# Performance work log

Hardware: AMD Instinct MI355X
Metric: run time of the kernel (lower is better)

Reference implementation:

```python
import jax, jax.numpy as jnp
import numpy as np

B, C, H, W = 4, 512, 64, 64
RED = 2
IC = C // RED  # inter_channels = 256


def _conv1x1(x, w, b):
    # mmcv ConvModule default: conv(+bias) then ReLU
    return jax.nn.relu(jnp.einsum('bchw,oc->bohw', x, w) + b[None, :, None, None])


def setup_inputs() -> dict:
    key = jax.random.key(0)
    ks = jax.random.split(key, 9)
    s_q = 0.02  # small init so exp(-dist) stays in a sane range
    return {
        'features': jax.random.normal(ks[0], (B, C, H, W), jnp.float32),
        'qw': jax.random.normal(ks[1], (IC, C), jnp.float32) * s_q,
        'qb': jnp.zeros((IC,), jnp.float32),
        'kw': jax.random.normal(ks[2], (IC, C), jnp.float32) * s_q,
        'kb': jnp.zeros((IC,), jnp.float32),
        'vw': jax.random.normal(ks[3], (C, C), jnp.float32) * s_q,
        'vb': jnp.zeros((C,), jnp.float32),
        'cw': jax.random.normal(ks[4], (IC, 2), jnp.float32) * s_q,
        'cb': jnp.zeros((IC,), jnp.float32),
    }


def reference(features, qw, qb, kw, kb, vw, vb, cw, cb):
    b, c, h, w = features.shape
    q = _conv1x1(features, qw, qb)   # [b, IC, h, w]
    k = _conv1x1(features, kw, kb)   # [b, IC, h, w]
    v = _conv1x1(features, vw, vb)   # [b, C,  h, w]

    # coordinate grid: channel 0 varies along w, channel 1 along h
    lin = jnp.linspace(-1.0, 1.0, h)
    A = jnp.broadcast_to(lin[None, :], (h, w))
    coord = jnp.broadcast_to(jnp.stack([A, A.T], axis=0)[None], (b, 2, h, w))
    cc = _conv1x1(coord, cw, cb)     # [b, IC, h, w]

    q = q + cc
    k = k + cc

    n = h * w
    Qf = q.reshape(b, -1, n).transpose(0, 2, 1)  # [b, n, IC]
    Kf = k.reshape(b, -1, n)                     # [b, IC, n]

    dots = jnp.einsum('bnc,bcm->bnm', Qf, Kf)    # [b, n, n]
    a_sq = jnp.sum(Qf * Qf, axis=-1)             # [b, n]
    b_sq = jnp.sum(Kf * Kf, axis=1)              # [b, n]
    D = a_sq[:, :, None] + b_sq[:, None, :] - 2.0 * dots
    S = jnp.exp(-D)
    S = S / (jnp.sum(S, axis=-1, keepdims=True) + 1e-14)

    Vf = v.reshape(b, c, n)                      # [b, C, n]
    out = jnp.einsum('bcn,bnm->bcm', Vf, S).reshape(b, c, h, w)
    return out + features
```

## Files before the change

kernel.cpp:

```cpp
#include <hip/hip_runtime.h>
#include <math.h>

#define BATCH 4
#define CH    512
#define ICH   256
#define NPIX  4096

typedef short short8 __attribute__((ext_vector_type(8)));
typedef float floatx4 __attribute__((ext_vector_type(4)));

#define BK   64
#define TS   136

static __device__ __forceinline__ unsigned short f2bf(float x) {
    union { float f; unsigned u; } v; v.f = x;
    unsigned r = (v.u + 0x7FFF + ((v.u >> 16) & 1)) >> 16;
    return (unsigned short)r;
}
static __device__ __forceinline__ float bf2f(unsigned short u) {
    union { unsigned u; float f; } v; v.u = ((unsigned)u) << 16; return v.f;
}
static __device__ __forceinline__ unsigned pack_bf(unsigned ue, unsigned uo) {
    return ((ue + 0x8000u) >> 16) | ((uo + 0x8000u) & 0xFFFF0000u);
}

static __device__ __forceinline__ void gld16(const unsigned short* g, unsigned short* l) {
    __builtin_amdgcn_global_load_lds(
        (const __attribute__((address_space(1))) unsigned int*)g,
        (__attribute__((address_space(3))) unsigned int*)l,
        16, 0, 0);
}

#define STAGE_TILE(L, M, row0, RS, k0)                                        \
    {                                                                         \
        int r_  = (it*32) + wid*8 + (lane >> 3);                              \
        int c_  = (lane & 7) ^ ((lane >> 3) & 7);                             \
        gld16(&(M)[(size_t)((row0) + r_)*(RS) + (k0) + c_*8],                 \
              &(L)[(it*32 + wid*8)*64]);                                      \
    }

#define STG64(L, M, row0, RS, k0, u)                                          \
    {                                                                         \
        int r_  = (u)*64 + wid*8 + (lane >> 3);                               \
        int c_  = (lane & 7) ^ ((lane >> 3) & 7);                             \
        gld16(&(M)[(size_t)((row0) + r_)*(RS) + (k0) + c_*8],                 \
              &(L)[((u)*64 + wid*8)*64]);                                     \
    }

#define FRAG(L, row, ks) \
    (*(const short8*)&(L)[(row)*64 + (((((ks)<<2) + quad) ^ (lo & 7)) << 3)])

__global__ __launch_bounds__(256)
void prep_w(const float* __restrict__ qw, const float* __restrict__ kw,
            const float* __restrict__ vw, unsigned short* __restrict__ Wb)
{
    int i = (blockIdx.x*256 + threadIdx.x) * 4;
    const float* src;
    int off;
    if (i < 256*512)            { src = qw; off = i; }
    else if (i < 512*512)       { src = kw; off = i - 256*512; }
    else                        { src = vw; off = i - 512*512; }
    float4 f = *(const float4*)&src[off];
    unsigned short pk[4] = { f2bf(f.x), f2bf(f.y), f2bf(f.z), f2bf(f.w) };
    *(uint2*)&Wb[i] = *(uint2*)pk;
}

__global__ __launch_bounds__(256)
void prep_ft(const float* __restrict__ feat, unsigned short* __restrict__ Ft)
{
    __shared__ unsigned short S[64][65];
    const int t = threadIdx.x;
    const int n0 = blockIdx.x * 64, c0 = blockIdx.y * 64, b = blockIdx.z;

    #pragma unroll
    for (int rep = 0; rep < 4; rep++) {
        int cl = rep*16 + (t >> 4), col4 = (t & 15) * 4;
        float4 f = *(const float4*)&feat[((size_t)b*CH + c0 + cl)*NPIX + n0 + col4];
        S[cl][col4 + 0] = f2bf(f.x);
        S[cl][col4 + 1] = f2bf(f.y);
        S[cl][col4 + 2] = f2bf(f.z);
        S[cl][col4 + 3] = f2bf(f.w);
    }
    __syncthreads();
    #pragma unroll
    for (int rep = 0; rep < 4; rep++) {
        int nn = rep*16 + (t >> 4), cq = t & 15;
        unsigned short h4[4];
        #pragma unroll
        for (int j = 0; j < 4; j++) h4[j] = S[cq*4 + j][nn];
        *(uint2*)&Ft[((size_t)b*NPIX + n0 + nn)*CH + c0 + cq*4] = *(uint2*)h4;
    }
}

__global__ __launch_bounds__(256)
void conv_mfma(const unsigned short* __restrict__ Ft,
               const unsigned short* __restrict__ Wb,
               const float* __restrict__ qb, const float* __restrict__ kb,
               const float* __restrict__ vb,
               const float* __restrict__ cw, const float* __restrict__ cb,
               unsigned short* __restrict__ Qt, unsigned short* __restrict__ Kt,
               unsigned short* __restrict__ Vt)
{
    __shared__ unsigned short SH[128*TS];
    unsigned short* L0 = SH;
    unsigned short* L2 = SH + 128*64;

    const int tid = threadIdx.x;
    const int wid = tid >> 6, lane = tid & 63, quad = lane >> 4, lo = lane & 15;
    const int n0 = blockIdx.x * 128;
    const int yb = blockIdx.y;
    const int bz = blockIdx.z;
    const int o_base = yb * 128;
    const int waveA = (wid >> 1) * 64, waveB = (wid & 1) * 64;
    const int is_v = (yb >= 4);
    const size_t fb = (size_t)bz*NPIX;

    floatx4 acc[4][4] = {};

    for (int k0 = 0; k0 < CH; k0 += BK) {
        #pragma unroll
        for (int it = 0; it < 4; it++) {
            STAGE_TILE(L0, Ft, fb + n0, CH, k0);
            STAGE_TILE(L2, Wb, o_base,  CH, k0);
        }
        __syncthreads();
        if (!is_v) {
            #pragma unroll
            for (int ks = 0; ks < 2; ks++) {
                short8 af[4], bw[4];
                #pragma unroll
                for (int i = 0; i < 4; i++) af[i] = FRAG(L0, waveA + i*16 + lo, ks);
                #pragma unroll
                for (int j = 0; j < 4; j++) bw[j] = FRAG(L2, waveB + j*16 + lo, ks);
                #pragma unroll
                for (int i = 0; i < 4; i++)
                    #pragma unroll
                    for (int j = 0; j < 4; j++)
                        acc[i][j] = __builtin_amdgcn_mfma_f32_16x16x32_bf16(af[i], bw[j], acc[i][j], 0, 0, 0);
            }
        } else {
            #pragma unroll
            for (int ks = 0; ks < 2; ks++) {
                short8 aw[4], bf[4];
                #pragma unroll
                for (int i = 0; i < 4; i++) aw[i] = FRAG(L2, waveA + i*16 + lo, ks);
                #pragma unroll
                for (int j = 0; j < 4; j++) bf[j] = FRAG(L0, waveB + j*16 + lo, ks);
                #pragma unroll
                for (int i = 0; i < 4; i++)
                    #pragma unroll
                    for (int j = 0; j < 4; j++)
                        acc[i][j] = __builtin_amdgcn_mfma_f32_16x16x32_bf16(aw[i], bf[j], acc[i][j], 0, 0, 0);
            }
        }
        __syncthreads();
    }

    const float step = 2.0f / 63.0f;
    if (!is_v) {
        const float* bp = (yb < 2) ? qb : kb;
        const int icg0 = (yb & 1) * 128;
        #pragma unroll
        for (int ib = 0; ib < 4; ib++) {
            int colL = waveB + ib*16 + lo;
            int ic = icg0 + colL;
            float bias = bp[ic];
            float cw0 = cw[ic*2+0], cw1 = cw[ic*2+1], cbv = cb[ic];
            #pragma unroll
            for (int ia = 0; ia < 4; ia++) {
                int rowL = waveA + ia*16 + quad*4;
                #pragma unroll
                for (int r = 0; r < 4; r++) {
                    int n = n0 + rowL + r;
                    float cx = -1.f + (n & 63)*step;
                    float cy = -1.f + (n >> 6)*step;
                    float v = fmaxf(acc[ia][ib][r] + bias, 0.f)
                            + fmaxf(cw0*cx + cw1*cy + cbv, 0.f);
                    unsigned u = __float_as_uint(v);
                    unsigned p = __shfl_xor(u, 1, 64);
                    if ((lo & 1) == 0)
                        *(unsigned*)&SH[(rowL + r)*TS + colL] = pack_bf(u, p);
                }
            }
        }
    } else {
        const int c_blk0 = (yb - 4) * 128;
        #pragma unroll
        for (int ia = 0; ia < 4; ia++) {
            int rowL = waveA + ia*16 + quad*4;
            #pragma unroll
            for (int r = 0; r < 4; r++) {
                float bias = vb[c_blk0 + rowL + r];
                #pragma unroll
                for (int ib = 0; ib < 4; ib++) {
                    int colL = waveB + ib*16 + lo;
                    float v = fmaxf(acc[ia][ib][r] + bias, 0.f);
                    unsigned u = __float_as_uint(v);
                    unsigned p = __shfl_xor(u, 1, 64);
                    if ((lo & 1) == 0)
                        *(unsigned*)&SH[(rowL + r)*TS + colL] = pack_bf(u, p);
                }
            }
        }
    }
    __syncthreads();

    unsigned short* dstp;
    int row0, rs, col0;
    if (!is_v) { dstp = ((yb < 2) ? Qt : Kt) + (size_t)bz*NPIX*ICH;
                 row0 = n0; rs = ICH; col0 = (yb & 1) * 128; }
    else       { dstp = Vt + (size_t)bz*CH*NPIX;
                 row0 = (yb - 4) * 128; rs = NPIX; col0 = n0; }
    #pragma unroll
    for (int it = 0; it < 8; it++) {
        int f = it*256 + tid;
        int row = f >> 4, col = (f & 15) * 8;
        uint4 v = *(const uint4*)&SH[row*TS + col];
        *(uint4*)&dstp[(size_t)(row0 + row)*rs + col0 + col] = v;
    }
}

__global__ __launch_bounds__(256)
void sqb_kernel(const unsigned short* __restrict__ Qt,
                const unsigned short* __restrict__ Kt,
                float* __restrict__ asq, float* __restrict__ bsq)
{
    int n = blockIdx.x*256 + threadIdx.x;
    int b = blockIdx.y;
    const unsigned short* q = Qt + ((size_t)b*NPIX + n)*ICH;
    const unsigned short* k = Kt + ((size_t)b*NPIX + n)*ICH;
    float qs = 0.f, ks = 0.f;
    #pragma unroll 4
    for (int i = 0; i < ICH/8; i++) {
        uint4 v = *(const uint4*)&q[i*8];
        const unsigned short* s = (const unsigned short*)&v;
        #pragma unroll
        for (int j = 0; j < 8; j++) { float a = bf2f(s[j]); qs += a*a; }
        uint4 w = *(const uint4*)&k[i*8];
        const unsigned short* t = (const unsigned short*)&w;
        #pragma unroll
        for (int j = 0; j < 8; j++) { float a = bf2f(t[j]); ks += a*a; }
    }
    asq[b*NPIX + n] = qs;
    bsq[b*NPIX + n] = ks;
}

__global__ __launch_bounds__(512)
void dots_mfma(const unsigned short* __restrict__ Kt_,
               const unsigned short* __restrict__ Qt_,
               const float* __restrict__ asq_, const float* __restrict__ bsq_,
               unsigned short* __restrict__ St_, float* __restrict__ rsum_,
               int b0)
{
    __shared__ unsigned short SH[128*TS];
    unsigned short* Al = SH;
    unsigned short* Bl = SH + 8192;

    const int tid = threadIdx.x;
    const int wid = tid >> 6, lane = tid & 63, quad = lane >> 4, lo = lane & 15;
    const int wm = wid >> 2;
    const int wn = wid & 3;
    const int m0 = blockIdx.x * 128, n0 = blockIdx.y * 128;
    const int bz = blockIdx.z, gb = b0 + bz;

    const unsigned short* Kt = Kt_ + (size_t)gb*NPIX*ICH;
    const unsigned short* Qt = Qt_ + (size_t)gb*NPIX*ICH;
    const float* asq = asq_ + (size_t)gb*NPIX;
    const float* bsq = bsq_ + (size_t)gb*NPIX;
    unsigned short* St = St_ + (size_t)bz*NPIX*NPIX;
    float* rsum = rsum_ + (size_t)gb*NPIX;

    floatx4 acc[4][2] = {};

    for (int k0 = 0; k0 < ICH; k0 += BK) {
        STG64(Al, Kt, m0, ICH, k0, 0);
        STG64(Al, Kt, m0, ICH, k0, 1);
        STG64(Bl, Qt, n0, ICH, k0, 0);
        STG64(Bl, Qt, n0, ICH, k0, 1);
        __syncthreads();
        #pragma unroll
        for (int ks = 0; ks < 2; ks++) {
            short8 a[4], bfr[2];
            #pragma unroll
            for (int i = 0; i < 4; i++) a[i]  = FRAG(Al, wm*64 + i*16 + lo, ks);
            #pragma unroll
            for (int j = 0; j < 2; j++) bfr[j] = FRAG(Bl, wn*32 + j*16 + lo, ks);
            #pragma unroll
            for (int i = 0; i < 4; i++)
                #pragma unroll
                for (int j = 0; j < 2; j++)
                    acc[i][j] = __builtin_amdgcn_mfma_f32_16x16x32_bf16(
                        a[i], bfr[j], acc[i][j], 0, 0, 0);
        }
        __syncthreads();
    }

    #pragma unroll
    for (int j = 0; j < 2; j++) {
        int nl = wn*32 + j*16 + lo;
        float aq = asq[n0 + nl];
        float colsum = 0.f;
        #pragma unroll
        for (int i = 0; i < 4; i++) {
            int mb = wm*64 + i*16 + quad*4;
            #pragma unroll
            for (int r = 0; r < 4; r++) {
                float d = aq + bsq[m0 + mb + r] - 2.f*acc[i][j][r];
                float sv = __expf(-d);
                colsum += sv;
                unsigned u = __float_as_uint(sv);
                unsigned p = __shfl_xor(u, 1, 64);
                if ((lo & 1) == 0)
                    *(unsigned*)&SH[(mb + r)*TS + nl] = pack_bf(u, p);
            }
        }
        colsum += __shfl_xor(colsum, 16, 64);
        colsum += __shfl_xor(colsum, 32, 64);
        if (quad == 0) atomicAdd(&rsum[n0 + nl], colsum);
    }
    __syncthreads();

    #pragma unroll
    for (int it = 0; it < 4; it++) {
        int f = it*512 + tid;
        int row = f >> 4, col = (f & 15) * 8;
        uint4 v = *(const uint4*)&SH[row*TS + col];
        *(uint4*)&St[(size_t)(m0 + row)*NPIX + n0 + col] = v;
    }
}

__global__ __launch_bounds__(256)
void vscale_kernel(const unsigned short* __restrict__ Vt,
                   const float* __restrict__ rsum,
                   unsigned short* __restrict__ Vp, int b0)
{
    int gb = b0 + blockIdx.y;
    size_t base = (size_t)gb*CH*NPIX + ((size_t)blockIdx.x*256 + threadIdx.x) * 8;
    int n = (int)(base & (NPIX - 1));
    const float* rs = rsum + (size_t)gb*NPIX;
    uint4 v = *(const uint4*)&Vt[base];
    const unsigned short* s = (const unsigned short*)&v;
    unsigned short pk[8];
    #pragma unroll
    for (int i = 0; i < 8; i++)
        pk[i] = f2bf(bf2f(s[i]) / (rs[n + i] + 1e-14f));
    *(uint4*)&Vp[base] = *(uint4*)pk;
}

#define PVBUF 24576
#define PVNT  (NPIX/BK)

__global__ __launch_bounds__(512)
void pv_mfma(const unsigned short* __restrict__ Vp_,
             const unsigned short* __restrict__ St_,
             const float* __restrict__ feat_, float* __restrict__ out_,
             int b0)
{
    __shared__ unsigned short SH3[3*PVBUF];
    const int tid = threadIdx.x;
    const int wid = tid >> 6, lane = tid & 63, quad = lane >> 4, lo = lane & 15;
    const int wm = wid >> 2;
    const int wn = wid & 3;
    const int m0 = blockIdx.x * 256, c0 = blockIdx.y * 128;
    const int bz = blockIdx.z, gb = b0 + bz;

    const unsigned short* Vp = Vp_ + (size_t)gb*CH*NPIX;
    const unsigned short* St = St_ + (size_t)bz*NPIX*NPIX;
    const float* feat = feat_ + (size_t)gb*CH*NPIX;
    float* out = out_ + (size_t)gb*CH*NPIX;

    floatx4 acc[4][4] = {};

    {
        unsigned short* A0 = SH3;            unsigned short* B0 = SH3 + 128*64;
        unsigned short* A1 = SH3 + PVBUF;    unsigned short* B1 = A1  + 128*64;
        STG64(A0, Vp, c0, NPIX, 0, 0);  STG64(A0, Vp, c0, NPIX, 0, 1);
        STG64(B0, St, m0, NPIX, 0, 0);  STG64(B0, St, m0, NPIX, 0, 1);
        STG64(B0, St, m0, NPIX, 0, 2);  STG64(B0, St, m0, NPIX, 0, 3);
        STG64(A1, Vp, c0, NPIX, BK, 0); STG64(A1, Vp, c0, NPIX, BK, 1);
        STG64(B1, St, m0, NPIX, BK, 0); STG64(B1, St, m0, NPIX, BK, 1);
        STG64(B1, St, m0, NPIX, BK, 2); STG64(B1, St, m0, NPIX, BK, 3);
    }
    asm volatile("s_waitcnt vmcnt(6)" ::: "memory");
    __builtin_amdgcn_s_barrier();

    int pc = 0, pn = 2;
    for (int s = 0; s < PVNT; ++s) {
        unsigned short* Ac = SH3 + pc*PVBUF;
        unsigned short* Bc = Ac + 128*64;
        unsigned short* An = SH3 + pn*PVBUF;
        unsigned short* Bn = An + 128*64;
        const int k2 = (s + 2) * BK;
        const bool stg = (s < PVNT - 2);

        short8 a0[2][4], b01[2][2];
        #pragma unroll
        for (int ks = 0; ks < 2; ks++) {
            #pragma unroll
            for (int i = 0; i < 4; i++)
                a0[ks][i] = FRAG(Ac, wm*64 + i*16 + lo, ks);
            #pragma unroll
            for (int j = 0; j < 2; j++)
                b01[ks][j] = FRAG(Bc, wn*64 + j*16 + lo, ks);
        }
        if (stg) {
            STG64(An, Vp, c0, NPIX, k2, 0);
            STG64(An, Vp, c0, NPIX, k2, 1);
            STG64(Bn, St, m0, NPIX, k2, 0);
        }
        __builtin_amdgcn_s_barrier();
        __builtin_amdgcn_s_setprio(1);
        #pragma unroll
        for (int ks = 0; ks < 2; ks++)
            #pragma unroll
            for (int i = 0; i < 4; i++)
                #pragma unroll
                for (int j = 0; j < 2; j++)
                    acc[i][j] = __builtin_amdgcn_mfma_f32_16x16x32_bf16(
                        a0[ks][i], b01[ks][j], acc[i][j], 0, 0, 0);
        __builtin_amdgcn_s_setprio(0);
        __builtin_amdgcn_s_barrier();

        short8 b23[2][2];
        #pragma unroll
        for (int ks = 0; ks < 2; ks++)
            #pragma unroll
            for (int j = 0; j < 2; j++)
                b23[ks][j] = FRAG(Bc, wn*64 + (j+2)*16 + lo, ks);
        if (stg) {
            STG64(Bn, St, m0, NPIX, k2, 1);
            STG64(Bn, St, m0, NPIX, k2, 2);
            STG64(Bn, St, m0, NPIX, k2, 3);
        }
        __builtin_amdgcn_s_barrier();
        __builtin_amdgcn_s_setprio(1);
        #pragma unroll
        for (int ks = 0; ks < 2; ks++)
            #pragma unroll
            for (int i = 0; i < 4; i++)
                #pragma unroll
                for (int j = 0; j < 2; j++)
                    acc[i][j+2] = __builtin_amdgcn_mfma_f32_16x16x32_bf16(
                        a0[ks][i], b23[ks][j], acc[i][j+2], 0, 0, 0);
        __builtin_amdgcn_s_setprio(0);

        if (s < PVNT - 2)       asm volatile("s_waitcnt vmcnt(6)" ::: "memory");
        else if (s == PVNT - 2) asm volatile("s_waitcnt vmcnt(0)" ::: "memory");
        __builtin_amdgcn_s_barrier();

        pc = (pc == 2) ? 0 : pc + 1;
        pn = (pn == 2) ? 0 : pn + 1;
    }

    #pragma unroll
    for (int i = 0; i < 4; i++) {
        int cr = c0 + wm*64 + i*16 + quad*4;
        #pragma unroll
        for (int r = 0; r < 4; r++) {
            size_t rowbase = (size_t)(cr + r)*NPIX;
            #pragma unroll
            for (int j = 0; j < 4; j++) {
                int m = m0 + wn*64 + j*16 + lo;
                out[rowbase + m] = acc[i][j][r] + feat[rowbase + m];
            }
        }
    }
}

extern "C" void kernel_launch(void* const* d_in, const int* in_sizes, int n_in,
                              void* d_out, int out_size, void* d_ws, size_t ws_size,
                              hipStream_t stream)
{
    const float* feat = (const float*)d_in[0];
    const float* qw   = (const float*)d_in[1];
    const float* qb   = (const float*)d_in[2];
    const float* kw   = (const float*)d_in[3];
    const float* kb   = (const float*)d_in[4];
    const float* vw   = (const float*)d_in[5];
    const float* vb   = (const float*)d_in[6];
    const float* cw   = (const float*)d_in[7];
    const float* cb   = (const float*)d_in[8];
    float* out = (float*)d_out;
    char* ws = (char*)d_ws;
    char* ws0 = ws;

    unsigned short* Ft  = (unsigned short*)ws;  ws += (size_t)BATCH*NPIX*CH*2;
    unsigned short* Wb  = (unsigned short*)ws;  ws += (size_t)1024*CH*2;
    unsigned short* Qt  = (unsigned short*)ws;  ws += (size_t)BATCH*NPIX*ICH*2;
    unsigned short* Kt  = (unsigned short*)ws;  ws += (size_t)BATCH*NPIX*ICH*2;
    unsigned short* Vt  = (unsigned short*)ws;  ws += (size_t)BATCH*CH*NPIX*2;
    unsigned short* Vp  = (unsigned short*)ws;  ws += (size_t)BATCH*CH*NPIX*2;
    float*         asq  = (float*)ws;           ws += (size_t)BATCH*NPIX*4;
    float*         bsq  = (float*)ws;           ws += (size_t)BATCH*NPIX*4;
    float*         rsum = (float*)ws;           ws += (size_t)BATCH*NPIX*4;
    unsigned short* St  = (unsigned short*)ws;

    const size_t st1 = (size_t)NPIX*NPIX*2;
    const size_t fixed = (size_t)(ws - ws0);
    const int nb = (ws_size >= fixed + (size_t)BATCH*st1) ? BATCH : 1;

    hipMemsetAsync(rsum, 0, (size_t)BATCH*NPIX*sizeof(float), stream);

    prep_w<<<dim3(512), 256, 0, stream>>>(qw, kw, vw, Wb);
    prep_ft<<<dim3(NPIX/64, CH/64, BATCH), 256, 0, stream>>>(feat, Ft);

    conv_mfma<<<dim3(NPIX/128, 8, BATCH), 256, 0, stream>>>(
        Ft, Wb, qb, kb, vb, cw, cb, Qt, Kt, Vt);

    sqb_kernel<<<dim3(NPIX/256, BATCH), 256, 0, stream>>>(Qt, Kt, asq, bsq);

    for (int b0 = 0; b0 < BATCH; b0 += nb) {
        dots_mfma<<<dim3(NPIX/128, NPIX/128, nb), 512, 0, stream>>>(
            Kt, Qt, asq, bsq, St, rsum, b0);
        vscale_kernel<<<dim3(CH*NPIX/(256*8), nb), 256, 0, stream>>>(
            Vt, rsum, Vp, b0);
        pv_mfma<<<dim3(NPIX/256, CH/128, nb), 512, 0, stream>>>(
            Vp, St, feat, out, b0);
    }
}
```

Baseline: 291.9 us.

## Load PV A-operand directly from global into registers, shrinking LDS buffers

The V operand of the PV GEMM is now read straight from global memory into registers, one K-step ahead and double-buffered in registers through a macro-unrolled loop pair. Only the S tiles go through the triple-buffered LDS ring, which shrinks each LDS stage and cuts LDS writes and reads for the A side. The vmcnt wait counts are retuned for the new mix of outstanding loads. The costs are higher register pressure and uncoalesced per-lane 16-byte global loads of V that may hit the caches less efficiently.

```diff
diff --git a/kernel.cpp b/kernel.cpp
--- a/kernel.cpp
+++ b/kernel.cpp
@@ -347,8 +347,70 @@
     *(uint4*)&Vp[base] = *(uint4*)pk;
 }
 
-#define PVBUF 24576
-#define PVNT  (NPIX/BK)
+#define PVB  16384
+#define PVNT (NPIX/BK)
+
+#define PV_STEP(s, AC, AN)                                                    \
+    {                                                                         \
+        unsigned short* Bc = SH3 + pc*PVB;                                    \
+        int pn_ = pc + 2; if (pn_ >= 3) pn_ -= 3;                             \
+        unsigned short* Bn = SH3 + pn_*PVB;                                   \
+        const int k2 = ((s) + 2) * BK;                                        \
+        const bool stg = ((s) < PVNT - 2);                                    \
+        short8 b01[2][2], b23[2][2];                                          \
+        _Pragma("unroll")                                                     \
+        for (int ks = 0; ks < 2; ks++)                                        \
+            _Pragma("unroll")                                                 \
+            for (int j = 0; j < 2; j++)                                       \
+                b01[ks][j] = FRAG(Bc, wn*64 + j*16 + lo, ks);                 \
+        if (stg) {                                                            \
+            STG64(Bn, St, m0, NPIX, k2, 0);                                   \
+            STG64(Bn, St, m0, NPIX, k2, 1);                                   \
+        }                                                                     \
+        if ((s) + 1 < PVNT) {                                                 \
+            _Pragma("unroll")                                                 \
+            for (int ks = 0; ks < 2; ks++)                                    \
+                _Pragma("unroll")                                             \
+                for (int i = 0; i < 4; i++)                                   \
+                    AN[ks][i] = *(const short8*)(ap[i] + ((s)+1)*64 + ks*32); \
+        }                                                                     \
+        __builtin_amdgcn_s_barrier();                                         \
+        __builtin_amdgcn_s_setprio(1);                                        \
+        _Pragma("unroll")                                                     \
+        for (int ks = 0; ks < 2; ks++)                                        \
+            _Pragma("unroll")                                                 \
+            for (int i = 0; i < 4; i++)                                       \
+                _Pragma("unroll")                                             \
+                for (int j = 0; j < 2; j++)                                   \
+                    acc[i][j] = __builtin_amdgcn_mfma_f32_16x16x32_bf16(      \
+                        AC[ks][i], b01[ks][j], acc[i][j], 0, 0, 0);           \
+        __builtin_amdgcn_s_setprio(0);                                        \
+        __builtin_amdgcn_s_barrier();                                         \
+        _Pragma("unroll")                                                     \
+        for (int ks = 0; ks < 2; ks++)                                        \
+            _Pragma("unroll")                                                 \
+            for (int j = 0; j < 2; j++)                                       \
+                b23[ks][j] = FRAG(Bc, wn*64 + (j+2)*16 + lo, ks);             \
+        if (stg) {                                                            \
+            STG64(Bn, St, m0, NPIX, k2, 2);                                   \
+            STG64(Bn, St, m0, NPIX, k2, 3);                                   \
+        }                                                                     \
+        __builtin_amdgcn_s_barrier();                                         \
+        __builtin_amdgcn_s_setprio(1);                                        \
+        _Pragma("unroll")                                                     \
+        for (int ks = 0; ks < 2; ks++)                                        \
+            _Pragma("unroll")                                                 \
+            for (int i = 0; i < 4; i++)                                       \
+                _Pragma("unroll")                                             \
+                for (int j = 0; j < 2; j++)                                   \
+                    acc[i][j+2] = __builtin_amdgcn_mfma_f32_16x16x32_bf16(    \
+                        AC[ks][i], b23[ks][j], acc[i][j+2], 0, 0, 0);         \
+        __builtin_amdgcn_s_setprio(0);                                        \
+        if (stg)                     asm volatile("s_waitcnt vmcnt(12)" ::: "memory"); \
+        else if ((s) == PVNT - 2)    asm volatile("s_waitcnt vmcnt(8)"  ::: "memory"); \
+        __builtin_amdgcn_s_barrier();                                         \
+        pc = pc + 1; if (pc >= 3) pc = 0;                                     \
+    }
 
 __global__ __launch_bounds__(512)
 void pv_mfma(const unsigned short* __restrict__ Vp_,
@@ -356,7 +418,7 @@
              const float* __restrict__ feat_, float* __restrict__ out_,
              int b0)
 {
-    __shared__ unsigned short SH3[3*PVBUF];
+    __shared__ unsigned short SH3[3*PVB];
     const int tid = threadIdx.x;
     const int wid = tid >> 6, lane = tid & 63, quad = lane >> 4, lo = lane & 15;
     const int wm = wid >> 2;
@@ -371,85 +433,29 @@
 
     floatx4 acc[4][4] = {};
 
-    {
-        unsigned short* A0 = SH3;            unsigned short* B0 = SH3 + 128*64;
-        unsigned short* A1 = SH3 + PVBUF;    unsigned short* B1 = A1  + 128*64;
-        STG64(A0, Vp, c0, NPIX, 0, 0);  STG64(A0, Vp, c0, NPIX, 0, 1);
-        STG64(B0, St, m0, NPIX, 0, 0);  STG64(B0, St, m0, NPIX, 0, 1);
-        STG64(B0, St, m0, NPIX, 0, 2);  STG64(B0, St, m0, NPIX, 0, 3);
-        STG64(A1, Vp, c0, NPIX, BK, 0); STG64(A1, Vp, c0, NPIX, BK, 1);
-        STG64(B1, St, m0, NPIX, BK, 0); STG64(B1, St, m0, NPIX, BK, 1);
-        STG64(B1, St, m0, NPIX, BK, 2); STG64(B1, St, m0, NPIX, BK, 3);
-    }
-    asm volatile("s_waitcnt vmcnt(6)" ::: "memory");
+    const unsigned short* ap[4];
+    #pragma unroll
+    for (int i = 0; i < 4; i++)
+        ap[i] = Vp + (size_t)(c0 + wm*64 + i*16 + lo)*NPIX + quad*8;
+
+    short8 aA[2][4], aB[2][4];
+
+    STG64(SH3,       St, m0, NPIX, 0,  0); STG64(SH3,       St, m0, NPIX, 0,  1);
+    STG64(SH3,       St, m0, NPIX, 0,  2); STG64(SH3,       St, m0, NPIX, 0,  3);
+    STG64(SH3 + PVB, St, m0, NPIX, BK, 0); STG64(SH3 + PVB, St, m0, NPIX, BK, 1);
+    STG64(SH3 + PVB, St, m0, NPIX, BK, 2); STG64(SH3 + PVB, St, m0, NPIX, BK, 3);
+    #pragma unroll
+    for (int ks = 0; ks < 2; ks++)
+        #pragma unroll
+        for (int i = 0; i < 4; i++)
+            aA[ks][i] = *(const short8*)(ap[i] + ks*32);
+    asm volatile("s_waitcnt vmcnt(0)" ::: "memory");
     __builtin_amdgcn_s_barrier();
 
-    int pc = 0, pn = 2;
-    for (int s = 0; s < PVNT; ++s) {
-        unsigned short* Ac = SH3 + pc*PVBUF;
-        unsigned short* Bc = Ac + 128*64;
-        unsigned short* An = SH3 + pn*PVBUF;
-        unsigned short* Bn = An + 128*64;
-        const int k2 = (s + 2) * BK;
-        const bool stg = (s < PVNT - 2);
-
-        short8 a0[2][4], b01[2][2];
-        #pragma unroll
-        for (int ks = 0; ks < 2; ks++) {
-            #pragma unroll
-            for (int i = 0; i < 4; i++)
-                a0[ks][i] = FRAG(Ac, wm*64 + i*16 + lo, ks);
-            #pragma unroll
-            for (int j = 0; j < 2; j++)
-                b01[ks][j] = FRAG(Bc, wn*64 + j*16 + lo, ks);
-        }
-        if (stg) {
-            STG64(An, Vp, c0, NPIX, k2, 0);
-            STG64(An, Vp, c0, NPIX, k2, 1);
-            STG64(Bn, St, m0, NPIX, k2, 0);
-        }
-        __builtin_amdgcn_s_barrier();
-        __builtin_amdgcn_s_setprio(1);
-        #pragma unroll
-        for (int ks = 0; ks < 2; ks++)
-            #pragma unroll
-            for (int i = 0; i < 4; i++)
-                #pragma unroll
-                for (int j = 0; j < 2; j++)
-                    acc[i][j] = __builtin_amdgcn_mfma_f32_16x16x32_bf16(
-                        a0[ks][i], b01[ks][j], acc[i][j], 0, 0, 0);
-        __builtin_amdgcn_s_setprio(0);
-        __builtin_amdgcn_s_barrier();
-
-        short8 b23[2][2];
-        #pragma unroll
-        for (int ks = 0; ks < 2; ks++)
-            #pragma unroll
-            for (int j = 0; j < 2; j++)
-                b23[ks][j] = FRAG(Bc, wn*64 + (j+2)*16 + lo, ks);
-        if (stg) {
-            STG64(Bn, St, m0, NPIX, k2, 1);
-            STG64(Bn, St, m0, NPIX, k2, 2);
-            STG64(Bn, St, m0, NPIX, k2, 3);
-        }
-        __builtin_amdgcn_s_barrier();
-        __builtin_amdgcn_s_setprio(1);
-        #pragma unroll
-        for (int ks = 0; ks < 2; ks++)
-            #pragma unroll
-            for (int i = 0; i < 4; i++)
-                #pragma unroll
-                for (int j = 0; j < 2; j++)
-                    acc[i][j+2] = __builtin_amdgcn_mfma_f32_16x16x32_bf16(
-                        a0[ks][i], b23[ks][j], acc[i][j+2], 0, 0, 0);
-        __builtin_amdgcn_s_setprio(0);
-
-        if (s < PVNT - 2)       asm volatile("s_waitcnt vmcnt(6)" ::: "memory");
-        else if (s == PVNT - 2) asm volatile("s_waitcnt vmcnt(0)" ::: "memory");
-        __builtin_amdgcn_s_barrier();
-
-        pc = (pc == 2) ? 0 : pc + 1;
-        pn = (pn == 2) ? 0 : pn + 1;
+    int pc = 0;
+    for (int t = 0; t < PVNT/2; ++t) {
+        PV_STEP(2*t,     aA, aB);
+        PV_STEP(2*t + 1, aB, aA);
     }
 
     #pragma unroll
```

After: 381.4 us. 30.7% more time.
